# Kernel optimization log

Hardware: AMD Instinct MI355X
Metric: run time of the kernel (lower is better)

## Reference

```python
import jax, jax.numpy as jnp
import numpy as np

N = 100000      # nodes
E = 3200000     # edges
G = 512         # graphs
F = 12          # num_features
NHID = 64
HGCN = NHID - 3   # 61, GCNConv output dim
EMB_OUT = 64 - F + 2  # 54


def _p(key, shape, scale):
    return jax.random.normal(key, shape, jnp.float32) * scale


def setup_inputs() -> dict:
    key = jax.random.key(0)
    ks = jax.random.split(key, 24)
    inp = {}
    inp["x"] = jax.random.normal(ks[0], (N, F), jnp.float32)
    inp["edge_index"] = jax.random.randint(ks[1], (2, E), 0, N)
    inp["batch"] = jnp.sort(jax.random.randint(ks[2], (N,), 0, G))
    inp["known_mask"] = jax.random.randint(ks[3], (E // 3,), 0, E)
    inp["unk_mask"] = jax.random.randint(ks[4], (E // 3,), 0, E)
    inp["obs_mask"] = jax.random.randint(ks[5], (E // 3,), 0, E)
    inp["fn_averages"] = jax.random.normal(ks[6], (G, 2), jnp.float32)
    inp["infection_rates"] = jax.random.normal(ks[7], (G, 1), jnp.float32)
    # parameters
    inp["msg_weights"] = jax.random.normal(ks[8], (3,), jnp.float32)
    inp["W_emb"] = _p(ks[9], (2, EMB_OUT), 0.5)
    inp["b_emb"] = jnp.zeros((EMB_OUT,), jnp.float32)
    inp["W_gcn"] = _p(ks[10], (64, HGCN), 0.125)
    inp["b_gcn"] = jnp.zeros((HGCN,), jnp.float32)
    inp["W_fn1"] = _p(ks[11], (3, 16), 0.5)
    inp["b_fn1"] = jnp.zeros((16,), jnp.float32)
    inp["W_fn2"] = _p(ks[12], (16, 3), 0.25)
    inp["b_fn2"] = jnp.zeros((3,), jnp.float32)
    inp["W_bb1"] = _p(ks[13], (NHID, NHID), 0.125)
    inp["b_bb1"] = jnp.zeros((NHID,), jnp.float32)
    inp["W_out"] = _p(ks[14], (NHID, 1), 0.125)
    inp["b_out"] = jnp.zeros((1,), jnp.float32)
    return inp


def reference(x, edge_index, batch, known_mask, unk_mask, obs_mask,
              fn_averages, infection_rates, msg_weights,
              W_emb, b_emb, W_gcn, b_gcn, W_fn1, b_fn1, W_fn2, b_fn2,
              W_bb1, b_bb1, W_out, b_out):
    gelu = lambda t: jax.nn.gelu(t, approximate=False)
    n = x.shape[0]
    e = edge_index.shape[1]
    g = fn_averages.shape[0]

    sp = jax.nn.softmax(msg_weights)
    ew = jnp.ones((e,), x.dtype)
    ew = ew.at[known_mask].set(sp[0]).at[unk_mask].set(sp[1]).at[obs_mask].set(sp[2])

    # node embedding: Linear on first 2 feats, concat rest -> (N, 64)
    h = jnp.concatenate([x[:, :2] @ W_emb + b_emb, x[:, 2:]], axis=1)

    # GCNConv(64 -> 61) with edge weights and self-loops
    h = h @ W_gcn                                  # (N, HGCN) transform first
    row, col = edge_index[0], edge_index[1]
    loop = jnp.arange(n)
    row_f = jnp.concatenate([row, loop])
    col_f = jnp.concatenate([col, loop])
    ew_f = jnp.concatenate([ew, jnp.ones((n,), ew.dtype)])
    deg = jax.ops.segment_sum(ew_f, col_f, num_segments=n)   # weighted in-degree
    dis = jnp.where(deg > 0, jax.lax.rsqrt(jnp.maximum(deg, 1e-12)), 0.0)
    norm = dis[row_f] * ew_f * dis[col_f]                    # (E+N,)
    out = jax.ops.segment_sum(norm[:, None] * h[row_f], col_f, num_segments=n)
    out = gelu(out + b_gcn)                                  # dropout = identity (eval)

    # global_add_pool over graphs
    pooled = jax.ops.segment_sum(out, batch, num_segments=g)  # (G, HGCN)

    # fn embeddings MLP on (fn_averages, infection_rate)
    extra = jnp.concatenate([fn_averages.reshape(-1, 2),
                             infection_rates.reshape(-1, 1)], axis=1)  # (G, 3)
    fn_e = gelu(extra @ W_fn1 + b_fn1) @ W_fn2 + b_fn2        # (G, 3)

    z = jnp.concatenate([pooled, fn_e], axis=1)               # (G, NHID)
    z = gelu(z @ W_bb1 + b_bb1)
    logits = z @ W_out + b_out                                # (G, 1)
    return logits
```

## Files before the change

### kernel.cpp

```cpp
#include <hip/hip_runtime.h>
#include <hip/hip_fp16.h>
#include <math.h>

#define F_IN 12
#define NHID 64
#define HGCN 61
#define EMB_OUT 54
#define SCAN_CH 1024
#define PART_R 8192
#define DEG_SCALE 32768.0f
#define W_SCALE 16384.0f

typedef unsigned int uint;
typedef unsigned short ushort;
typedef unsigned char uchar;

__device__ __forceinline__ float gelu_exact(float v) {
    return 0.5f * v * (1.0f + erff(v * 0.70710678118654752440f));
}

__device__ __forceinline__ void atomic_add_f32(float* p, float v) {
    unsafeAtomicAdd(p, v);
}

__global__ __launch_bounds__(256) void k1_hist_prep(
        const int* __restrict__ ei, uint* __restrict__ H, uchar* __restrict__ wclass,
        const float* __restrict__ msg_w, const float* __restrict__ W_emb,
        const float* __restrict__ b_emb, const float* __restrict__ W_gcn,
        uint* __restrict__ spq, uint* __restrict__ sq15,
        float* __restrict__ W_eff, float* __restrict__ b_eff,
        int E, int NB, int NBLK) {
    __shared__ uint hist[512];
    __shared__ float ssp[4];
    int blk = blockIdx.x, t = threadIdx.x;
    hist[t] = 0; hist[t + 256] = 0;
    if (blk == 0 && t == 0) {
        float m = fmaxf(msg_w[0], fmaxf(msg_w[1], msg_w[2]));
        float e0 = expf(msg_w[0] - m), e1 = expf(msg_w[1] - m), e2 = expf(msg_w[2] - m);
        float s = e0 + e1 + e2;
        ssp[0] = 1.0f; ssp[1] = e0 / s; ssp[2] = e1 / s; ssp[3] = e2 / s;
    }
    __syncthreads();
    if (blk == 0) {
        if (t < 4) {
            spq[t]  = __float2uint_rn(ssp[t] * DEG_SCALE);
            sq15[t] = __float2uint_rn(ssp[t] * W_SCALE);
        }
        if (t < HGCN) {
            float be = 0.f, w0 = 0.f, w1 = 0.f;
            for (int k = 0; k < EMB_OUT; ++k) {
                float g = W_gcn[k * HGCN + t];
                be += b_emb[k] * g;
                w0 += W_emb[k] * g;
                w1 += W_emb[EMB_OUT + k] * g;
            }
            b_eff[t] = be;
            W_eff[0 * 64 + t] = w0;
            W_eff[1 * 64 + t] = w1;
            for (int f = 2; f < F_IN; ++f)
                W_eff[f * 64 + t] = W_gcn[(EMB_OUT + f - 2) * HGCN + t];
        }
    }
    int lo = blk * PART_R, hi = min(lo + PART_R, E);
    for (int i = lo + t; i < hi; i += 256) {
        wclass[i] = 0;
        atomicAdd(&hist[((uint)ei[E + i]) >> 8], 1u);
    }
    __syncthreads();
    for (int b = t; b < NB; b += 256) H[(size_t)b * NBLK + blk] = hist[b];
}

__global__ void set_mask_u8(uchar* __restrict__ wclass, const int* __restrict__ mask,
                            uchar v, int n) {
    int i = blockIdx.x * blockDim.x + threadIdx.x;
    if (i < n) wclass[mask[i]] = v;
}

__global__ void scan_partial_kernel(const int* __restrict__ cnt, int* __restrict__ startv,
                                    int* __restrict__ bsum, int n) {
    __shared__ int s[256];
    int t = threadIdx.x;
    int base = blockIdx.x * SCAN_CH + t * 4;
    int v0 = (base + 0 < n) ? cnt[base + 0] : 0;
    int v1 = (base + 1 < n) ? cnt[base + 1] : 0;
    int v2 = (base + 2 < n) ? cnt[base + 2] : 0;
    int v3 = (base + 3 < n) ? cnt[base + 3] : 0;
    int loc = v0 + v1 + v2 + v3;
    s[t] = loc;
    __syncthreads();
    for (int off = 1; off < 256; off <<= 1) {
        int u = (t >= off) ? s[t - off] : 0;
        __syncthreads();
        s[t] += u;
        __syncthreads();
    }
    int ex = s[t] - loc;
    if (t == 255) bsum[blockIdx.x] = s[255];
    if (base + 0 < n) startv[base + 0] = ex;
    if (base + 1 < n) startv[base + 1] = ex + v0;
    if (base + 2 < n) startv[base + 2] = ex + v0 + v1;
    if (base + 3 < n) startv[base + 3] = ex + v0 + v1 + v2;
}

__global__ void scan_add_kernel(int* __restrict__ startv, const int* __restrict__ bsum, int n) {
    __shared__ int soff;
    int b = blockIdx.x;
    if (threadIdx.x == 0) {
        int q = (b * 256) / SCAN_CH;
        int acc = 0;
        for (int j = 0; j < q; ++j) acc += bsum[j];
        soff = acc;
    }
    __syncthreads();
    int i = b * 256 + threadIdx.x;
    if (i < n) startv[i] += soff;
}

__global__ __launch_bounds__(256) void k3_partition(
        const int* __restrict__ ei, const uchar* __restrict__ wclass,
        const uint* __restrict__ Hs, uint* __restrict__ recSorted,
        int E, int NB, int NBLK) {
    __shared__ uint recs[PART_R];
    __shared__ ushort sbkt[PART_R];
    __shared__ uint hist[512];
    __shared__ uint scanA[512];
    __shared__ uint scanB[512];
    __shared__ int  gbase[512];
    __shared__ uint cursor[512];
    int blk = blockIdx.x, t = threadIdx.x;
    int lo = blk * PART_R, hi = min(lo + PART_R, E);
    int cntTot = hi - lo;
    hist[t] = 0; hist[t + 256] = 0;
    __syncthreads();
    for (int i = lo + t; i < hi; i += 256)
        atomicAdd(&hist[((uint)ei[E + i]) >> 8], 1u);
    __syncthreads();
    uint* src = scanA; uint* dst = scanB;
    src[t] = hist[t]; src[t + 256] = hist[t + 256];
    __syncthreads();
    for (int off = 1; off < 512; off <<= 1) {
        dst[t]       = src[t]       + ((t >= off)       ? src[t - off]       : 0u);
        dst[t + 256] = src[t + 256] + ((t + 256 >= off) ? src[t + 256 - off] : 0u);
        __syncthreads();
        uint* tmp = src; src = dst; dst = tmp;
    }
    uint l0 = (t == 0) ? 0u : src[t - 1];
    uint l1 = src[t + 255];
    cursor[t] = l0; cursor[t + 256] = l1;
    if (t < NB)       gbase[t]       = (int)Hs[(size_t)t * NBLK + blk]         - (int)l0;
    if (t + 256 < NB) gbase[t + 256] = (int)Hs[(size_t)(t + 256) * NBLK + blk] - (int)l1;
    __syncthreads();
    for (int i = lo + t; i < hi; i += 256) {
        uint row = (uint)ei[i];
        uint col = (uint)ei[E + i];
        uint b = col >> 8;
        uint rec = (row << 10) | ((col & 255u) << 2) | (uint)wclass[i];
        uint slot = atomicAdd(&cursor[b], 1u);
        recs[slot] = rec;
        sbkt[slot] = (ushort)b;
    }
    __syncthreads();
    for (int s = t; s < cntTot; s += 256)
        recSorted[gbase[sbkt[s]] + s] = recs[s];
}

__global__ __launch_bounds__(256) void k2_stats(
        const uint* __restrict__ recSorted, const uint* __restrict__ Hs,
        const uint* __restrict__ spq,
        uint* __restrict__ cnt, uint* __restrict__ startv, float* __restrict__ dis,
        int E, int NB, int NBLK, int n_nodes) {
    __shared__ uint hcnt[256], hdeg[256], sA[256], sB[256];
    __shared__ uint sq[4];
    int b = blockIdx.x, t = threadIdx.x;
    hcnt[t] = 0; hdeg[t] = 0;
    if (t < 4) sq[t] = spq[t];
    __syncthreads();
    uint lo = Hs[(size_t)b * NBLK];
    uint hi = (b + 1 < NB) ? Hs[(size_t)(b + 1) * NBLK] : (uint)E;
    for (uint i = lo + t; i < hi; i += 256) {
        uint r = recSorted[i];
        atomicAdd(&hcnt[(r >> 2) & 255u], 1u);
        atomicAdd(&hdeg[(r >> 2) & 255u], sq[r & 3u]);
    }
    __syncthreads();
    uint* src = sA; uint* dst = sB;
    src[t] = hcnt[t];
    __syncthreads();
    for (int off = 1; off < 256; off <<= 1) {
        dst[t] = src[t] + ((t >= off) ? src[t - off] : 0u);
        __syncthreads();
        uint* tmp = src; src = dst; dst = tmp;
    }
    uint excl = (t == 0) ? 0u : src[t - 1];
    int node = (b << 8) + t;
    if (node < n_nodes) {
        cnt[node] = hcnt[t];
        startv[node] = lo + excl;
        float deg = (float)hdeg[t] * (1.0f / DEG_SCALE) + 1.0f;
        dis[node] = rsqrtf(deg);
    }
}

__global__ __launch_bounds__(256) void k4_payload(
        const uint* __restrict__ recSorted, const uint* __restrict__ Hs,
        const uint* __restrict__ sq15, const uint* __restrict__ startv,
        uint* __restrict__ payload, int E, int NB, int NBLK, int n_nodes) {
    __shared__ uint cur[256];
    __shared__ uint wq[4];
    int b = blockIdx.x, t = threadIdx.x;
    int node = (b << 8) + t;
    cur[t] = (node < n_nodes) ? startv[node] : 0u;
    if (t < 4) wq[t] = sq15[t];
    __syncthreads();
    uint lo = Hs[(size_t)b * NBLK];
    uint hi = (b + 1 < NB) ? Hs[(size_t)(b + 1) * NBLK] : (uint)E;
    for (uint i = lo + t; i < hi; i += 256) {
        uint r = recSorted[i];
        uint pos = atomicAdd(&cur[(r >> 2) & 255u], 1u);
        payload[pos] = ((r >> 10) << 15) | wq[r & 3u];
    }
}

__global__ void h2_kernel(const float* __restrict__ x, const float* __restrict__ W_eff,
                          const float* __restrict__ b_eff, const float* __restrict__ dis,
                          __half* __restrict__ h2, float* __restrict__ pooled, int g64,
                          int n_nodes) {
    int gid = blockIdx.x * 256 + threadIdx.x;
    if (gid < g64) pooled[gid] = 0.0f;
    int node = blockIdx.x * 4 + (threadIdx.x >> 6);
    int d = threadIdx.x & 63;
    if (node >= n_nodes) return;
    float v = 0.f;
    if (d < HGCN) {
        v = b_eff[d];
#pragma unroll
        for (int f = 0; f < F_IN; ++f)
            v += x[node * F_IN + f] * W_eff[f * 64 + d];
        v *= dis[node];
    }
    h2[node * 64 + d] = __float2half(v);
}

__global__ void gather_pool_kernel(const uint* __restrict__ payload,
                                   const uint* __restrict__ startv, const uint* __restrict__ cnt,
                                   const float* __restrict__ dis,
                                   const __half2* __restrict__ h2v,
                                   const float* __restrict__ b_gcn, const int* __restrict__ batch,
                                   float* __restrict__ pooled, int n_nodes) {
    int node = blockIdx.x * 4 + (threadIdx.x >> 6);
    int lane = threadIdx.x & 63;
    int g = lane >> 5;
    int sub = lane & 31;
    if (node >= n_nodes) return;
    int s = (int)startv[node];
    int m = (int)cnt[node];
    const float inv = 1.0f / W_SCALE;
    float accx = 0.f, accy = 0.f;
    if (g == 0) {
        float2 hv = __half22float2(h2v[node * 32 + sub]);
        accx = hv.x;
        accy = hv.y;
    }
    for (int j0 = 0; j0 < m; j0 += 64) {
        uint p = 0;
        if (j0 + lane < m) p = payload[s + j0 + lane];
        int lim = min(64, m - j0);
        int npairs = (lim + 1) >> 1;
        int k = 0;
        for (; k + 8 <= npairs; k += 8) {
            uint p0 = __shfl(p, 2 * (k + 0) + g);
            uint p1 = __shfl(p, 2 * (k + 1) + g);
            uint p2 = __shfl(p, 2 * (k + 2) + g);
            uint p3 = __shfl(p, 2 * (k + 3) + g);
            uint p4 = __shfl(p, 2 * (k + 4) + g);
            uint p5 = __shfl(p, 2 * (k + 5) + g);
            uint p6 = __shfl(p, 2 * (k + 6) + g);
            uint p7 = __shfl(p, 2 * (k + 7) + g);
            float2 h0 = __half22float2(h2v[(p0 >> 15) * 32 + sub]);
            float2 h1 = __half22float2(h2v[(p1 >> 15) * 32 + sub]);
            float2 h2f = __half22float2(h2v[(p2 >> 15) * 32 + sub]);
            float2 h3 = __half22float2(h2v[(p3 >> 15) * 32 + sub]);
            float2 h4 = __half22float2(h2v[(p4 >> 15) * 32 + sub]);
            float2 h5 = __half22float2(h2v[(p5 >> 15) * 32 + sub]);
            float2 h6 = __half22float2(h2v[(p6 >> 15) * 32 + sub]);
            float2 h7 = __half22float2(h2v[(p7 >> 15) * 32 + sub]);
            float w0 = (float)(p0 & 32767u) * inv;
            float w1 = (float)(p1 & 32767u) * inv;
            float w2 = (float)(p2 & 32767u) * inv;
            float w3 = (float)(p3 & 32767u) * inv;
            float w4 = (float)(p4 & 32767u) * inv;
            float w5 = (float)(p5 & 32767u) * inv;
            float w6 = (float)(p6 & 32767u) * inv;
            float w7 = (float)(p7 & 32767u) * inv;
            accx += w0 * h0.x; accy += w0 * h0.y;
            accx += w1 * h1.x; accy += w1 * h1.y;
            accx += w2 * h2f.x; accy += w2 * h2f.y;
            accx += w3 * h3.x; accy += w3 * h3.y;
            accx += w4 * h4.x; accy += w4 * h4.y;
            accx += w5 * h5.x; accy += w5 * h5.y;
            accx += w6 * h6.x; accy += w6 * h6.y;
            accx += w7 * h7.x; accy += w7 * h7.y;
        }
        for (; k < npairs; ++k) {
            uint pk = __shfl(p, 2 * k + g);
            float2 hk = __half22float2(h2v[(pk >> 15) * 32 + sub]);
            float wk = (float)(pk & 32767u) * inv;
            accx += wk * hk.x; accy += wk * hk.y;
        }
    }
    accx += __shfl_xor(accx, 32);
    accy += __shfl_xor(accy, 32);
    int d = 2 * sub + g;
    float val = (g ? accy : accx) * dis[node];
    if (d < HGCN) {
        float v = gelu_exact(val + b_gcn[d]);
        atomic_add_f32(&pooled[batch[node] * 64 + d], v);
    }
}

__global__ void final_kernel(const float* __restrict__ pooled,
                             const float* __restrict__ fn_avg,
                             const float* __restrict__ inf_rate,
                             const float* __restrict__ W_fn1, const float* __restrict__ b_fn1,
                             const float* __restrict__ W_fn2, const float* __restrict__ b_fn2,
                             const float* __restrict__ W_bb1, const float* __restrict__ b_bb1,
                             const float* __restrict__ W_out, const float* __restrict__ b_out,
                             float* __restrict__ logits) {
    __shared__ float z[64];
    __shared__ float t1[16];
    int g = blockIdx.x;
    int t = threadIdx.x;
    if (t < HGCN) z[t] = pooled[g * 64 + t];
    float e0 = fn_avg[g * 2], e1 = fn_avg[g * 2 + 1], e2 = inf_rate[g];
    if (t < 16) {
        float a = e0 * W_fn1[t] + e1 * W_fn1[16 + t] + e2 * W_fn1[32 + t] + b_fn1[t];
        t1[t] = gelu_exact(a);
    }
    __syncthreads();
    if (t < 3) {
        float a = b_fn2[t];
#pragma unroll
        for (int k = 0; k < 16; ++k) a += t1[k] * W_fn2[k * 3 + t];
        z[HGCN + t] = a;
    }
    __syncthreads();
    float acc = b_bb1[t];
#pragma unroll 8
    for (int k = 0; k < 64; ++k) acc += z[k] * W_bb1[k * 64 + t];
    float p = gelu_exact(acc) * W_out[t];
#pragma unroll
    for (int off = 32; off > 0; off >>= 1) p += __shfl_down(p, off);
    if (t == 0) logits[g] = p + b_out[0];
}

extern "C" void kernel_launch(void* const* d_in, const int* in_sizes, int n_in,
                              void* d_out, int out_size, void* d_ws, size_t ws_size,
                              hipStream_t stream) {
    const float* x        = (const float*)d_in[0];
    const int*   ei       = (const int*)d_in[1];
    const int*   batch    = (const int*)d_in[2];
    const int*   known    = (const int*)d_in[3];
    const int*   unk      = (const int*)d_in[4];
    const int*   obs      = (const int*)d_in[5];
    const float* fn_avg   = (const float*)d_in[6];
    const float* inf_rate = (const float*)d_in[7];
    const float* msg_w    = (const float*)d_in[8];
    const float* W_emb    = (const float*)d_in[9];
    const float* b_emb    = (const float*)d_in[10];
    const float* W_gcn    = (const float*)d_in[11];
    const float* b_gcn    = (const float*)d_in[12];
    const float* W_fn1    = (const float*)d_in[13];
    const float* b_fn1    = (const float*)d_in[14];
    const float* W_fn2    = (const float*)d_in[15];
    const float* b_fn2    = (const float*)d_in[16];
    const float* W_bb1    = (const float*)d_in[17];
    const float* b_bb1    = (const float*)d_in[18];
    const float* W_out    = (const float*)d_in[19];
    const float* b_out    = (const float*)d_in[20];
    float* logits = (float*)d_out;

    const int n_nodes = in_sizes[0] / F_IN;
    const int E       = in_sizes[1] / 2;
    const int nk = in_sizes[3], nu = in_sizes[4], no = in_sizes[5];
    const int G = in_sizes[6] / 2;

    const int NB   = (n_nodes + 255) >> 8;
    const int NBLK = (E + PART_R - 1) / PART_R;
    const int L    = NB * NBLK;
    const int nbL  = (L + SCAN_CH - 1) / SCAN_CH;

    char* ws = (char*)d_ws;
    size_t off = 0;
    auto alloc = [&](size_t bytes) -> void* {
        void* p = ws + off;
        off += (bytes + 255) & ~size_t(255);
        return p;
    };
    uchar*  wclass    = (uchar*)alloc(sizeof(uchar) * (size_t)E);
    uint*   recSorted = (uint*)alloc(sizeof(uint) * (size_t)E);
    uint*   H         = (uint*)alloc(sizeof(uint) * (size_t)L);
    uint*   Hs        = (uint*)alloc(sizeof(uint) * (size_t)L);
    int*    bsum      = (int*)alloc(sizeof(int) * (size_t)(nbL + 1));
    __half* h2        = (__half*)alloc(sizeof(__half) * (size_t)n_nodes * 64);
    uint*   payload   = (uint*)alloc(sizeof(uint) * (size_t)E);
    uint*   cntv      = (uint*)alloc(sizeof(uint) * (size_t)n_nodes);
    uint*   startv    = (uint*)alloc(sizeof(uint) * (size_t)n_nodes);
    float*  dis       = (float*)alloc(sizeof(float) * (size_t)n_nodes);
    float*  pooled    = (float*)alloc(sizeof(float) * (size_t)G * 64);
    float*  W_eff     = (float*)alloc(sizeof(float) * F_IN * 64);
    float*  b_eff     = (float*)alloc(sizeof(float) * 64);
    uint*   spq       = (uint*)alloc(sizeof(uint) * 4);
    uint*   sq15      = (uint*)alloc(sizeof(uint) * 4);

    k1_hist_prep<<<NBLK, 256, 0, stream>>>(ei, H, wclass, msg_w, W_emb, b_emb, W_gcn,
                                           spq, sq15, W_eff, b_eff, E, NB, NBLK);
    set_mask_u8<<<(nk + 255) / 256, 256, 0, stream>>>(wclass, known, 1, nk);
    set_mask_u8<<<(nu + 255) / 256, 256, 0, stream>>>(wclass, unk, 2, nu);
    set_mask_u8<<<(no + 255) / 256, 256, 0, stream>>>(wclass, obs, 3, no);
    scan_partial_kernel<<<nbL, 256, 0, stream>>>((const int*)H, (int*)Hs, bsum, L);
    scan_add_kernel<<<(L + 255) / 256, 256, 0, stream>>>((int*)Hs, bsum, L);
    k3_partition<<<NBLK, 256, 0, stream>>>(ei, wclass, Hs, recSorted, E, NB, NBLK);
    k2_stats<<<NB, 256, 0, stream>>>(recSorted, Hs, spq, cntv, startv, dis, E, NB, NBLK, n_nodes);
    h2_kernel<<<(n_nodes + 3) / 4, 256, 0, stream>>>(x, W_eff, b_eff, dis, h2, pooled,
                                                     G * 64, n_nodes);
    k4_payload<<<NB, 256, 0, stream>>>(recSorted, Hs, sq15, startv, payload, E, NB, NBLK, n_nodes);
    gather_pool_kernel<<<(n_nodes + 3) / 4, 256, 0, stream>>>(payload, startv, cntv, dis,
                                                              (const __half2*)h2, b_gcn, batch,
                                                              pooled, n_nodes);
    final_kernel<<<G, 64, 0, stream>>>(pooled, fn_avg, inf_rate, W_fn1, b_fn1,
                                       W_fn2, b_fn2, W_bb1, b_bb1, W_out, b_out, logits);
}
```

Measured before the change: 228.8 us.

## Reuse k1 histogram in partition and fuse stats with payload scatter

The partition kernel now reads the per-block bucket histogram already computed by k1 instead of rebuilding it with shared-memory atomics over the column indices. The stats and payload kernels are merged, so each bucket's sorted records are read by one block that computes counts, degrees and starts and then scatters payload using in-block cursors. This removes one launch, a full re-read of the column array, and a global startv read. The merged kernel does serial passes within a block, and reusing H assumes its layout matches what the partition expects.

New measurement: 216.4 us (median of 2 runs). -5.4%, faster.

```diff
diff --git a/kernel.cpp b/kernel.cpp
--- a/kernel.cpp
+++ b/kernel.cpp
@@ -118,11 +118,10 @@
 
 __global__ __launch_bounds__(256) void k3_partition(
         const int* __restrict__ ei, const uchar* __restrict__ wclass,
-        const uint* __restrict__ Hs, uint* __restrict__ recSorted,
-        int E, int NB, int NBLK) {
+        const uint* __restrict__ H, const uint* __restrict__ Hs,
+        uint* __restrict__ recSorted, int E, int NB, int NBLK) {
     __shared__ uint recs[PART_R];
     __shared__ ushort sbkt[PART_R];
-    __shared__ uint hist[512];
     __shared__ uint scanA[512];
     __shared__ uint scanB[512];
     __shared__ int  gbase[512];
@@ -130,13 +129,10 @@
     int blk = blockIdx.x, t = threadIdx.x;
     int lo = blk * PART_R, hi = min(lo + PART_R, E);
     int cntTot = hi - lo;
-    hist[t] = 0; hist[t + 256] = 0;
-    __syncthreads();
-    for (int i = lo + t; i < hi; i += 256)
-        atomicAdd(&hist[((uint)ei[E + i]) >> 8], 1u);
-    __syncthreads();
+    uint h0 = (t < NB)       ? H[(size_t)t * NBLK + blk]         : 0u;
+    uint h1 = (t + 256 < NB) ? H[(size_t)(t + 256) * NBLK + blk] : 0u;
     uint* src = scanA; uint* dst = scanB;
-    src[t] = hist[t]; src[t + 256] = hist[t + 256];
+    src[t] = h0; src[t + 256] = h1;
     __syncthreads();
     for (int off = 1; off < 512; off <<= 1) {
         dst[t]       = src[t]       + ((t >= off)       ? src[t - off]       : 0u);
@@ -164,16 +160,17 @@
         recSorted[gbase[sbkt[s]] + s] = recs[s];
 }
 
-__global__ __launch_bounds__(256) void k2_stats(
+__global__ __launch_bounds__(256) void k2k4(
         const uint* __restrict__ recSorted, const uint* __restrict__ Hs,
-        const uint* __restrict__ spq,
+        const uint* __restrict__ spq, const uint* __restrict__ sq15,
         uint* __restrict__ cnt, uint* __restrict__ startv, float* __restrict__ dis,
-        int E, int NB, int NBLK, int n_nodes) {
+        uint* __restrict__ payload, int E, int NB, int NBLK, int n_nodes) {
     __shared__ uint hcnt[256], hdeg[256], sA[256], sB[256];
-    __shared__ uint sq[4];
+    __shared__ uint cur[256];
+    __shared__ uint sq[4], wq[4];
     int b = blockIdx.x, t = threadIdx.x;
     hcnt[t] = 0; hdeg[t] = 0;
-    if (t < 4) sq[t] = spq[t];
+    if (t < 4) { sq[t] = spq[t]; wq[t] = sq15[t]; }
     __syncthreads();
     uint lo = Hs[(size_t)b * NBLK];
     uint hi = (b + 1 < NB) ? Hs[(size_t)(b + 1) * NBLK] : (uint)E;
@@ -199,21 +196,8 @@
         float deg = (float)hdeg[t] * (1.0f / DEG_SCALE) + 1.0f;
         dis[node] = rsqrtf(deg);
     }
-}
-
-__global__ __launch_bounds__(256) void k4_payload(
-        const uint* __restrict__ recSorted, const uint* __restrict__ Hs,
-        const uint* __restrict__ sq15, const uint* __restrict__ startv,
-        uint* __restrict__ payload, int E, int NB, int NBLK, int n_nodes) {
-    __shared__ uint cur[256];
-    __shared__ uint wq[4];
-    int b = blockIdx.x, t = threadIdx.x;
-    int node = (b << 8) + t;
-    cur[t] = (node < n_nodes) ? startv[node] : 0u;
-    if (t < 4) wq[t] = sq15[t];
-    __syncthreads();
-    uint lo = Hs[(size_t)b * NBLK];
-    uint hi = (b + 1 < NB) ? Hs[(size_t)(b + 1) * NBLK] : (uint)E;
+    cur[t] = lo + excl;
+    __syncthreads();
     for (uint i = lo + t; i < hi; i += 256) {
         uint r = recSorted[i];
         uint pos = atomicAdd(&cur[(r >> 2) & 255u], 1u);
@@ -419,11 +403,11 @@
     set_mask_u8<<<(no + 255) / 256, 256, 0, stream>>>(wclass, obs, 3, no);
     scan_partial_kernel<<<nbL, 256, 0, stream>>>((const int*)H, (int*)Hs, bsum, L);
     scan_add_kernel<<<(L + 255) / 256, 256, 0, stream>>>((int*)Hs, bsum, L);
-    k3_partition<<<NBLK, 256, 0, stream>>>(ei, wclass, Hs, recSorted, E, NB, NBLK);
-    k2_stats<<<NB, 256, 0, stream>>>(recSorted, Hs, spq, cntv, startv, dis, E, NB, NBLK, n_nodes);
+    k3_partition<<<NBLK, 256, 0, stream>>>(ei, wclass, H, Hs, recSorted, E, NB, NBLK);
+    k2k4<<<NB, 256, 0, stream>>>(recSorted, Hs, spq, sq15, cntv, startv, dis, payload,
+                                 E, NB, NBLK, n_nodes);
     h2_kernel<<<(n_nodes + 3) / 4, 256, 0, stream>>>(x, W_eff, b_eff, dis, h2, pooled,
                                                      G * 64, n_nodes);
-    k4_payload<<<NB, 256, 0, stream>>>(recSorted, Hs, sq15, startv, payload, E, NB, NBLK, n_nodes);
     gather_pool_kernel<<<(n_nodes + 3) / 4, 256, 0, stream>>>(payload, startv, cntv, dis,
                                                               (const __half2*)h2, b_gcn, batch,
                                                               pooled, n_nodes);
```
